# Performance work log

Measured on AMD Instinct MI355X. Metric: run time of the kernel, lower is better.

## Reference

```python
import jax, jax.numpy as jnp
import numpy as np

BN_EPS = 1e-5


def _bn(x, gamma, beta):
    # BatchNorm1d in training mode: batch mean, biased variance
    m = jnp.mean(x, axis=0)
    v = jnp.var(x, axis=0)
    return (x - m) * jax.lax.rsqrt(v + BN_EPS) * gamma + beta


def _gin_rel(h_src, h_dst, src, dst, W1, W2, g1, b1, g2, b2):
    # GINConv (eps=0): sum-aggregate src features onto dst, add self feature
    n_dst = h_dst.shape[0]
    agg = jax.ops.segment_sum(h_src[src], dst, num_segments=n_dst)  # [N_dst, d]
    x = h_dst + agg
    # MLP: Linear -> BN -> ReLU -> Linear  (both Linears bias=False)
    h = jax.nn.relu(_bn(x @ W1, g1, b1)) @ W2
    # GINBase: BN -> ReLU
    return jax.nn.relu(_bn(h, g2, b2))


def setup_inputs() -> dict:
    key = jax.random.key(0)
    ks = jax.random.split(key, 12)
    N_U, N_I, E, D = 50000, 50000, 640000, 128
    s = 1.0 / np.sqrt(D)
    inp = {
        "h_user": jax.random.normal(ks[0], (N_U, D), jnp.float32),
        "h_item": jax.random.normal(ks[1], (N_I, D), jnp.float32),
        "src_rates": jax.random.randint(ks[2], (E,), 0, N_U, jnp.int32),
        "dst_rates": jax.random.randint(ks[3], (E,), 0, N_I, jnp.int32),
        "src_rev": jax.random.randint(ks[4], (E,), 0, N_I, jnp.int32),
        "dst_rev": jax.random.randint(ks[5], (E,), 0, N_U, jnp.int32),
        "W1_rates": jax.random.normal(ks[6], (D, D), jnp.float32) * s,
        "W2_rates": jax.random.normal(ks[7], (D, D), jnp.float32) * s,
        "g1_rates": jnp.ones((D,), jnp.float32),
        "b1_rates": jnp.zeros((D,), jnp.float32),
        "g2_rates": jnp.ones((D,), jnp.float32),
        "b2_rates": jnp.zeros((D,), jnp.float32),
        "W1_rev": jax.random.normal(ks[8], (D, D), jnp.float32) * s,
        "W2_rev": jax.random.normal(ks[9], (D, D), jnp.float32) * s,
        "g1_rev": jnp.ones((D,), jnp.float32),
        "b1_rev": jnp.zeros((D,), jnp.float32),
        "g2_rev": jnp.ones((D,), jnp.float32),
        "b2_rev": jnp.zeros((D,), jnp.float32),
    }
    return inp


def reference(h_user, h_item, src_rates, dst_rates, src_rev, dst_rev,
              W1_rates, W2_rates, g1_rates, b1_rates, g2_rates, b2_rates,
              W1_rev, W2_rev, g1_rev, b1_rev, g2_rev, b2_rev):
    # relation 'rates': user -> item; relation 'rated_by': item -> user
    out_item = _gin_rel(h_user, h_item, src_rates, dst_rates,
                        W1_rates, W2_rates, g1_rates, b1_rates, g2_rates, b2_rates)
    out_user = _gin_rel(h_item, h_user, src_rev, dst_rev,
                        W1_rev, W2_rev, g1_rev, b1_rev, g2_rev, b2_rev)
    # HeteroGraphConv sums per dst type; one relation per dst type here.
    # GINLayer squeezes each output (no-op for 2D tensors).
    return (out_user, out_item)
```

## Files before the change

kernel.cpp:

```cpp
#include <hip/hip_runtime.h>

#define D 128
#define NBUK 4
#define NCHF 128
#define FILL_FINE 1024
#define MAXT 4
#define FUSE_GX 256
static constexpr float BN_EPS = 1e-5f;

typedef __attribute__((ext_vector_type(8))) short short8;
typedef __attribute__((ext_vector_type(4))) float f32x4;

__device__ __forceinline__ unsigned short f2bf(float f)
{
    unsigned u = __builtin_bit_cast(unsigned, f);
    unsigned r = u + 0x7fffu + ((u >> 16) & 1u);
    return (unsigned short)(r >> 16);
}
__device__ __forceinline__ float bflo(unsigned u)
{
    return __builtin_bit_cast(float, u << 16);
}
__device__ __forceinline__ float bfhi(unsigned u)
{
    return __builtin_bit_cast(float, u & 0xffff0000u);
}

struct CsrRel {
    const int* src; const int* dst;
    int* counts; int* offsets; int* bsum; int* perm;
    unsigned char* rank8; unsigned* pc;
    int E; int N; int nscan;
};
struct GatherRel {
    const unsigned short* hb;
    const unsigned short* hbd;
    const int* offsets; const int* perm;
    unsigned short* x; int N;
};
struct FusedRel {
    const unsigned short* X;
    const unsigned short* Wt1;
    const unsigned short* Wt2;
    const float* g1; const float* b1; const float* g2; const float* b2;
    float* st;
    float* out;
    int N; int ntiles;
};

__global__ __launch_bounds__(256) void prep_kernel(
    const float* __restrict__ hu, const float* __restrict__ hi,
    unsigned short* __restrict__ bu, unsigned short* __restrict__ bi8,
    int nu8, int ni8,
    const float* __restrict__ Wa, const float* __restrict__ Wb,
    const float* __restrict__ Wc, const float* __restrict__ Wd,
    unsigned short* __restrict__ wt, float* __restrict__ stats,
    int* __restrict__ bar)
{
    const int t = threadIdx.x;
    if (blockIdx.x < 64) {
        const int wsel = blockIdx.x >> 4;
        const float* W = wsel == 0 ? Wa : wsel == 1 ? Wb : wsel == 2 ? Wc : Wd;
        unsigned short* out = wt + (size_t)wsel * D * D;
        const int tile = blockIdx.x & 15;
        const int k0 = (tile >> 2) * 32, n0 = (tile & 3) * 32;
        __shared__ float s[32][33];
        const int r = t >> 3, c = (t & 7) * 4;
        float4 v = *reinterpret_cast<const float4*>(W + (size_t)(k0 + r) * D + n0 + c);
        s[r][c] = v.x; s[r][c + 1] = v.y; s[r][c + 2] = v.z; s[r][c + 3] = v.w;
        __syncthreads();
        unsigned lo = (unsigned)f2bf(s[c][r]) | ((unsigned)f2bf(s[c + 1][r]) << 16);
        unsigned hi = (unsigned)f2bf(s[c + 2][r]) | ((unsigned)f2bf(s[c + 3][r]) << 16);
        *reinterpret_cast<uint2*>(out + (size_t)(n0 + r) * D + k0 + c) =
            make_uint2(lo, hi);
        return;
    }
    if (blockIdx.x == 64) {
        reinterpret_cast<float4*>(stats)[t] = make_float4(0.f, 0.f, 0.f, 0.f);
        if (t < 8) bar[t] = 0;
        return;
    }
    int i = (blockIdx.x - 65) * 256 + t;
    if (i >= nu8 + ni8) return;
    const float* s; unsigned short* d; int o;
    if (i < nu8) { s = hu; d = bu; o = i; }
    else         { s = hi; d = bi8; o = i - nu8; }
    float4 v0 = reinterpret_cast<const float4*>(s)[o * 2];
    float4 v1 = reinterpret_cast<const float4*>(s)[o * 2 + 1];
    uint4 r;
    r.x = (unsigned)f2bf(v0.x) | ((unsigned)f2bf(v0.y) << 16);
    r.y = (unsigned)f2bf(v0.z) | ((unsigned)f2bf(v0.w) << 16);
    r.z = (unsigned)f2bf(v1.x) | ((unsigned)f2bf(v1.y) << 16);
    r.w = (unsigned)f2bf(v1.z) | ((unsigned)f2bf(v1.w) << 16);
    reinterpret_cast<uint4*>(d)[o] = r;
}

__global__ __launch_bounds__(256) void hist_kernel(CsrRel r0, CsrRel r1)
{
    CsrRel r = blockIdx.y ? r1 : r0;
    extern __shared__ unsigned h4[];
    const int t = threadIdx.x;
    const int c = blockIdx.x;
    const int CE = (r.E + NCHF - 1) / NCHF;
    const int e0 = c * CE;
    const int e1 = min(e0 + CE, r.E);
    const int bw4 = (r.N + 3) >> 2;

    for (int i = t; i < bw4; i += 256) h4[i] = 0u;
    __syncthreads();
    for (int e = e0 + t; e < e1; e += 256) {
        int d = r.dst[e];
        unsigned sh = (unsigned)(d & 3) * 8u;
        unsigned old = atomicAdd(&h4[d >> 2], 1u << sh);
        r.rank8[e] = (unsigned char)((old >> sh) & 0xffu);
    }
    __syncthreads();
    unsigned* out = r.pc + (size_t)c * bw4;
    for (int i = t; i < bw4; i += 256) out[i] = h4[i];
}

__global__ __launch_bounds__(256) void chunkpfx_kernel(CsrRel r0, CsrRel r1)
{
    CsrRel r = blockIdx.y ? r1 : r0;
    __shared__ unsigned lds[NCHF * 256];
    const int t = threadIdx.x;
    const int j = blockIdx.x * 256 + t;
    const int bw4 = (r.N + 3) >> 2;
    int s = 0;
    if (j < bw4) {
        const unsigned* base = r.pc + j;
#pragma unroll 4
        for (int c = 0; c < NCHF; ++c)
            lds[c * 256 + t] = base[(size_t)c * bw4];
        unsigned s0 = 0, s1 = 0, s2 = 0, s3 = 0;
        for (int c = 0; c < NCHF; ++c) {
            unsigned v = lds[c * 256 + t];
            lds[c * 256 + t] = s0 | (s1 << 8) | (s2 << 16) | (s3 << 24);
            s0 += v & 0xffu;
            s1 += (v >> 8) & 0xffu;
            s2 += (v >> 16) & 0xffu;
            s3 += v >> 24;
        }
        unsigned* wb = r.pc + j;
#pragma unroll 4
        for (int c = 0; c < NCHF; ++c)
            wb[(size_t)c * bw4] = lds[c * 256 + t];
        int d0 = 4 * j;
        r.counts[d0] = (int)s0;
        if (d0 + 1 < r.N) r.counts[d0 + 1] = (int)s1;
        if (d0 + 2 < r.N) r.counts[d0 + 2] = (int)s2;
        if (d0 + 3 < r.N) r.counts[d0 + 3] = (int)s3;
        s = (int)(s0 + s1 + s2 + s3);
    }
    __shared__ int red[256];
    red[t] = s;
    __syncthreads();
    for (int off = 128; off > 0; off >>= 1) {
        if (t < off) red[t] += red[t + off];
        __syncthreads();
    }
    if (t == 0) r.bsum[blockIdx.x] = red[0];
}

__global__ __launch_bounds__(256) void scan_offsets_kernel(CsrRel rr0, CsrRel rr1)
{
    CsrRel r = blockIdx.y ? rr1 : rr0;
    if ((int)blockIdx.x >= r.nscan) return;
    __shared__ int pb[64];
    __shared__ int part[256];
    const int t = threadIdx.x;
    if (t == 0) {
        int run = 0;
        for (int i = 0; i < r.nscan; ++i) { pb[i] = run; run += r.bsum[i]; }
    }
    const int d0 = blockIdx.x * 1024 + t * 4;
    int v0 = 0, v1 = 0, v2 = 0, v3 = 0;
    if (d0 + 3 < r.N) {
        int4 q = *reinterpret_cast<const int4*>(r.counts + d0);
        v0 = q.x; v1 = q.y; v2 = q.z; v3 = q.w;
    } else {
        if (d0 < r.N) v0 = r.counts[d0];
        if (d0 + 1 < r.N) v1 = r.counts[d0 + 1];
        if (d0 + 2 < r.N) v2 = r.counts[d0 + 2];
        if (d0 + 3 < r.N) v3 = r.counts[d0 + 3];
    }
    int s = v0 + v1 + v2 + v3;
    part[t] = s;
    __syncthreads();
    for (int off = 1; off < 256; off <<= 1) {
        int tmp = (t >= off) ? part[t - off] : 0;
        __syncthreads();
        part[t] += tmp;
        __syncthreads();
    }
    int excl = part[t] - s + pb[blockIdx.x];
    int o0 = excl, o1 = o0 + v0, o2 = o1 + v1, o3 = o2 + v2;
    if (d0 + 3 < r.N) {
        *reinterpret_cast<int4*>(r.offsets + d0) = make_int4(o0, o1, o2, o3);
    } else {
        if (d0 < r.N) r.offsets[d0] = o0;
        if (d0 + 1 < r.N) r.offsets[d0 + 1] = o1;
        if (d0 + 2 < r.N) r.offsets[d0 + 2] = o2;
        if (d0 + 3 < r.N) r.offsets[d0 + 3] = o3;
    }
    if (d0 < r.N && d0 + 4 >= r.N) r.offsets[r.N] = excl + s;
}

__global__ __launch_bounds__(256) void fill_kernel(CsrRel rr0, CsrRel rr1)
{
    CsrRel r = blockIdx.y ? rr1 : rr0;
    const int b = blockIdx.x & (NBUK - 1);
    const int fc = blockIdx.x >> 2;
    const int f0 = fc * FILL_FINE;
    if (f0 >= r.E) return;
    const int f1 = min(f0 + FILL_FINE, r.E);
    const int bw = (r.N + NBUK - 1) / NBUK;
    const int lo = b * bw;
    const int hi = min(lo + bw, r.N);
    const int CE = (r.E + NCHF - 1) / NCHF;
    const int c0 = f0 / CE;
    const int cb = (c0 + 1) * CE;
    const int bw4 = (r.N + 3) >> 2;
    const unsigned* pcb0 = r.pc + (size_t)c0 * bw4;
    const unsigned* pcb1 = pcb0 + bw4;
    for (int e = f0 + threadIdx.x; e < f1; e += 256) {
        int d = r.dst[e];
        if (d >= lo && d < hi) {
            const unsigned* pcc = (e >= cb) ? pcb1 : pcb0;
            unsigned sh = (unsigned)(d & 3) * 8u;
            int px = (int)((pcc[d >> 2] >> sh) & 0xffu);
            r.perm[r.offsets[d] + px + (int)r.rank8[e]] = r.src[e];
        }
    }
}

__global__ __launch_bounds__(256) void gather_agg_kernel(GatherRel g0, GatherRel g1)
{
    GatherRel g = blockIdx.y ? g1 : g0;
    int row = blockIdx.x * 4 + (threadIdx.x >> 6);
    row = __builtin_amdgcn_readfirstlane(row);
    if (row >= g.N) return;
    const int c = (threadIdx.x & 63) * 2;
    const int beg = g.offsets[row], end = g.offsets[row + 1];
    unsigned us = *reinterpret_cast<const unsigned*>(g.hbd + (size_t)row * D + c);
    float2 acc = make_float2(bflo(us), bfhi(us));
    const unsigned short* hb = g.hb;
    int i = beg;
    for (; i + 7 < end; i += 8) {
        unsigned u[8];
#pragma unroll
        for (int k = 0; k < 8; ++k) {
            int s = g.perm[i + k];
            u[k] = *reinterpret_cast<const unsigned*>(hb + (size_t)s * D + c);
        }
        float ax = 0.f, ay = 0.f;
#pragma unroll
        for (int k = 0; k < 8; ++k) { ax += bflo(u[k]); ay += bfhi(u[k]); }
        acc.x += ax;
        acc.y += ay;
    }
    if (i + 3 < end) {
        int s0 = g.perm[i], s1 = g.perm[i + 1];
        int s2 = g.perm[i + 2], s3 = g.perm[i + 3];
        unsigned u0 = *reinterpret_cast<const unsigned*>(hb + (size_t)s0 * D + c);
        unsigned u1 = *reinterpret_cast<const unsigned*>(hb + (size_t)s1 * D + c);
        unsigned u2 = *reinterpret_cast<const unsigned*>(hb + (size_t)s2 * D + c);
        unsigned u3 = *reinterpret_cast<const unsigned*>(hb + (size_t)s3 * D + c);
        acc.x += (bflo(u0) + bflo(u1)) + (bflo(u2) + bflo(u3));
        acc.y += (bfhi(u0) + bfhi(u1)) + (bfhi(u2) + bfhi(u3));
        i += 4;
    }
    for (; i < end; ++i) {
        unsigned u = *reinterpret_cast<const unsigned*>(hb + (size_t)g.perm[i] * D + c);
        acc.x += bflo(u);
        acc.y += bfhi(u);
    }
    unsigned o = (unsigned)f2bf(acc.x) | ((unsigned)f2bf(acc.y) << 16);
    *reinterpret_cast<unsigned*>(g.x + (size_t)row * D + c) = o;
}

__device__ __forceinline__ unsigned bnpack(unsigned u, float sLo, float sHi,
                                           float bLo, float bHi)
{
    float lo = fmaxf(fmaf(bflo(u), sLo, bLo), 0.f);
    float hi = fmaxf(fmaf(bfhi(u), sHi, bHi), 0.f);
    return (unsigned)f2bf(lo) | ((unsigned)f2bf(hi) << 16);
}

__device__ __forceinline__ void rel_barrier(int* ctr)
{
    __syncthreads();
    if (threadIdx.x == 0) {
        __hip_atomic_fetch_add(ctr, 1, __ATOMIC_RELAXED, __HIP_MEMORY_SCOPE_AGENT);
        while (__hip_atomic_load(ctr, __ATOMIC_RELAXED, __HIP_MEMORY_SCOPE_AGENT)
               < FUSE_GX)
            __builtin_amdgcn_s_sleep(2);
        int v = __hip_atomic_load(ctr, __ATOMIC_ACQUIRE, __HIP_MEMORY_SCOPE_AGENT);
        asm volatile("" :: "s"(v));
    }
    __syncthreads();
}

__device__ __forceinline__ float ld_atomic(const float* p)
{
    return __hip_atomic_load(p, __ATOMIC_RELAXED, __HIP_MEMORY_SCOPE_AGENT);
}

__global__ __launch_bounds__(256, 2) void fused_mlp_kernel(FusedRel q0, FusedRel q1,
                                                           int* bar)
{
    FusedRel q = blockIdx.y ? q1 : q0;
    int* bA = bar + blockIdx.y * 2;
    __shared__ unsigned short ylds[MAXT * 64 * D];
    __shared__ float s_sc[D], s_bi[D];
    __shared__ float ssum[4][D], ssq[4][D];
    char* yb = reinterpret_cast<char*>(ylds);

    const int t = threadIdx.x;
    const int w = t >> 6;
    const int l = t & 63;
    const int lr = l & 15;
    const int lk = (l >> 4) << 3;

    uint4 wf[4][8];
    float ps[8], pq[8];

#pragma unroll
    for (int kk = 0; kk < 4; ++kk)
#pragma unroll
        for (int n = 0; n < 8; ++n)
            wf[kk][n] = *reinterpret_cast<const uint4*>(
                q.Wt1 + (size_t)(n * 16 + lr) * D + kk * 32 + lk);
#pragma unroll
    for (int n = 0; n < 8; ++n) { ps[n] = 0.f; pq[n] = 0.f; }

    for (int mt = 0; mt < MAXT; ++mt) {
        int tile = (int)blockIdx.x + mt * FUSE_GX;
        if (tile >= q.ntiles) break;
        f32x4 acc[8];
#pragma unroll
        for (int n = 0; n < 8; ++n) acc[n] = (f32x4){0.f, 0.f, 0.f, 0.f};
        const int arow = tile * 64 + w * 16 + lr;
#pragma unroll
        for (int kk = 0; kk < 4; ++kk) {
            uint4 a4 = make_uint4(0u, 0u, 0u, 0u);
            if (arow < q.N)
                a4 = *reinterpret_cast<const uint4*>(
                    q.X + (size_t)arow * D + kk * 32 + lk);
            short8 a = __builtin_bit_cast(short8, a4);
#pragma unroll
            for (int n = 0; n < 8; ++n)
                acc[n] = __builtin_amdgcn_mfma_f32_16x16x32_bf16(
                    a, __builtin_bit_cast(short8, wf[kk][n]), acc[n], 0, 0, 0);
        }
        const int lrow = w * 16 + ((l >> 4) << 2);
#pragma unroll
        for (int n = 0; n < 8; ++n) {
#pragma unroll
            for (int j = 0; j < 4; ++j) {
                float v = acc[n][j];
                ps[n] += v;
                pq[n] += v * v;
                int row = lrow + j;
                int by = (((row << 8) + ((n * 16 + lr) << 1)) ^ ((row & 7) << 4));
                *reinterpret_cast<unsigned short*>(yb + mt * 16384 + by) = f2bf(v);
            }
        }
    }
#pragma unroll
    for (int n = 0; n < 8; ++n) {
        ps[n] += __shfl_xor(ps[n], 16); ps[n] += __shfl_xor(ps[n], 32);
        pq[n] += __shfl_xor(pq[n], 16); pq[n] += __shfl_xor(pq[n], 32);
    }
    if (l < 16) {
#pragma unroll
        for (int n = 0; n < 8; ++n) {
            ssum[w][n * 16 + l] = ps[n];
            ssq[w][n * 16 + l]  = pq[n];
        }
    }
    __syncthreads();
    if (t < D) {
        atomicAdd(&q.st[t], ssum[0][t] + ssum[1][t] + ssum[2][t] + ssum[3][t]);
        atomicAdd(&q.st[D + t], ssq[0][t] + ssq[1][t] + ssq[2][t] + ssq[3][t]);
    }
    rel_barrier(bA);

    if (t < D) {
        float inv_n = 1.f / (float)q.N;
        float mean = ld_atomic(&q.st[t]) * inv_n;
        float var = fmaxf(ld_atomic(&q.st[D + t]) * inv_n - mean * mean, 0.f);
        float s = q.g1[t] * rsqrtf(var + BN_EPS);
        s_sc[t] = s;
        s_bi[t] = q.b1[t] - mean * s;
    }
    __syncthreads();
#pragma unroll
    for (int kk = 0; kk < 4; ++kk)
#pragma unroll
        for (int n = 0; n < 8; ++n)
            wf[kk][n] = *reinterpret_cast<const uint4*>(
                q.Wt2 + (size_t)(n * 16 + lr) * D + kk * 32 + lk);
#pragma unroll
    for (int n = 0; n < 8; ++n) { ps[n] = 0.f; pq[n] = 0.f; }

    for (int mt = 0; mt < MAXT; ++mt) {
        int tile = (int)blockIdx.x + mt * FUSE_GX;
        if (tile >= q.ntiles) break;
        f32x4 acc[8];
#pragma unroll
        for (int n = 0; n < 8; ++n) acc[n] = (f32x4){0.f, 0.f, 0.f, 0.f};
        const int yrow = w * 16 + lr;
        const int grow = tile * 64 + yrow;
#pragma unroll
        for (int kk = 0; kk < 4; ++kk) {
            uint4 a4 = make_uint4(0u, 0u, 0u, 0u);
            if (grow < q.N) {
                int by = (((yrow << 8) + ((kk * 32 + lk) << 1)) ^ ((yrow & 7) << 4));
                a4 = *reinterpret_cast<const uint4*>(yb + mt * 16384 + by);
                const int kb = kk * 32 + lk;
                float4 s0 = *reinterpret_cast<const float4*>(&s_sc[kb]);
                float4 s1 = *reinterpret_cast<const float4*>(&s_sc[kb + 4]);
                float4 b0 = *reinterpret_cast<const float4*>(&s_bi[kb]);
                float4 b1 = *reinterpret_cast<const float4*>(&s_bi[kb + 4]);
                a4.x = bnpack(a4.x, s0.x, s0.y, b0.x, b0.y);
                a4.y = bnpack(a4.y, s0.z, s0.w, b0.z, b0.w);
                a4.z = bnpack(a4.z, s1.x, s1.y, b1.x, b1.y);
                a4.w = bnpack(a4.w, s1.z, s1.w, b1.z, b1.w);
            }
            short8 a = __builtin_bit_cast(short8, a4);
#pragma unroll
            for (int n = 0; n < 8; ++n)
                acc[n] = __builtin_amdgcn_mfma_f32_16x16x32_bf16(
                    a, __builtin_bit_cast(short8, wf[kk][n]), acc[n], 0, 0, 0);
        }
        const int lrow = w * 16 + ((l >> 4) << 2);
#pragma unroll
        for (int n = 0; n < 8; ++n) {
#pragma unroll
            for (int j = 0; j < 4; ++j) {
                float v = acc[n][j];
                ps[n] += v;
                pq[n] += v * v;
                int row = lrow + j;
                int by = (((row << 8) + ((n * 16 + lr) << 1)) ^ ((row & 7) << 4));
                *reinterpret_cast<unsigned short*>(yb + mt * 16384 + by) = f2bf(v);
            }
        }
    }
#pragma unroll
    for (int n = 0; n < 8; ++n) {
        ps[n] += __shfl_xor(ps[n], 16); ps[n] += __shfl_xor(ps[n], 32);
        pq[n] += __shfl_xor(pq[n], 16); pq[n] += __shfl_xor(pq[n], 32);
    }
    __syncthreads();
    if (l < 16) {
#pragma unroll
        for (int n = 0; n < 8; ++n) {
            ssum[w][n * 16 + l] = ps[n];
            ssq[w][n * 16 + l]  = pq[n];
        }
    }
    __syncthreads();
    if (t < D) {
        atomicAdd(&q.st[2 * D + t], ssum[0][t] + ssum[1][t] + ssum[2][t] + ssum[3][t]);
        atomicAdd(&q.st[3 * D + t], ssq[0][t] + ssq[1][t] + ssq[2][t] + ssq[3][t]);
    }
    rel_barrier(bA + 1);

    if (t < D) {
        float inv_n = 1.f / (float)q.N;
        float mean = ld_atomic(&q.st[2 * D + t]) * inv_n;
        float var = fmaxf(ld_atomic(&q.st[3 * D + t]) * inv_n - mean * mean, 0.f);
        float s = q.g2[t] * rsqrtf(var + BN_EPS);
        s_sc[t] = s;
        s_bi[t] = q.b2[t] - mean * s;
    }
    __syncthreads();
    const float sc0 = s_sc[2 * l], sc1 = s_sc[2 * l + 1];
    const float bi0 = s_bi[2 * l], bi1 = s_bi[2 * l + 1];
    for (int mt = 0; mt < MAXT; ++mt) {
        int tile = (int)blockIdx.x + mt * FUSE_GX;
        if (tile >= q.ntiles) break;
#pragma unroll
        for (int rr = 0; rr < 16; ++rr) {
            int row = w * 16 + rr;
            int grow = tile * 64 + row;
            if (grow >= q.N) break;
            int by = (((row << 8) + (l << 2)) ^ ((row & 7) << 4));
            unsigned u = *reinterpret_cast<const unsigned*>(yb + mt * 16384 + by);
            float2 o;
            o.x = fmaxf(fmaf(bflo(u), sc0, bi0), 0.f);
            o.y = fmaxf(fmaf(bfhi(u), sc1, bi1), 0.f);
            *reinterpret_cast<float2*>(q.out + (size_t)grow * D + 2 * l) = o;
        }
    }
}

extern "C" void kernel_launch(void* const* d_in, const int* in_sizes, int n_in,
                              void* d_out, int out_size, void* d_ws, size_t ws_size,
                              hipStream_t stream)
{
    const float* h_user   = (const float*)d_in[0];
    const float* h_item   = (const float*)d_in[1];
    const int* src_rates  = (const int*)d_in[2];
    const int* dst_rates  = (const int*)d_in[3];
    const int* src_rev    = (const int*)d_in[4];
    const int* dst_rev    = (const int*)d_in[5];
    const float* W1_rates = (const float*)d_in[6];
    const float* W2_rates = (const float*)d_in[7];
    const float* g1_rates = (const float*)d_in[8];
    const float* b1_rates = (const float*)d_in[9];
    const float* g2_rates = (const float*)d_in[10];
    const float* b2_rates = (const float*)d_in[11];
    const float* W1_rev   = (const float*)d_in[12];
    const float* W2_rev   = (const float*)d_in[13];
    const float* g1_rev   = (const float*)d_in[14];
    const float* b1_rev   = (const float*)d_in[15];
    const float* g2_rev   = (const float*)d_in[16];
    const float* b2_rev   = (const float*)d_in[17];

    const int n_user = in_sizes[0] / D;
    const int n_item = in_sizes[1] / D;
    const int E1 = in_sizes[2];
    const int E2 = in_sizes[4];

    const int bw4_0 = (n_item + 3) >> 2;
    const int bw4_1 = (n_user + 3) >> 2;

    char* p = (char*)d_ws;
    auto alloc = [&](size_t bytes) {
        char* q = p;
        p += (bytes + 255) & ~(size_t)255;
        return q;
    };
    unsigned short* hbu = (unsigned short*)alloc((size_t)n_user * D * 2);
    unsigned short* hbi = (unsigned short*)alloc((size_t)n_item * D * 2);
    unsigned short* xz0 = (unsigned short*)alloc((size_t)n_item * D * 2);
    unsigned short* xz1 = (unsigned short*)alloc((size_t)n_user * D * 2);
    unsigned short* wt  = (unsigned short*)alloc((size_t)4 * D * D * 2);
    float* stats   = (float*)alloc((size_t)8 * D * 4);
    int* bar       = (int*)alloc((size_t)8 * 4);
    int* counts0   = (int*)alloc((size_t)n_item * 4);
    int* counts1   = (int*)alloc((size_t)n_user * 4);
    int* offsets0  = (int*)alloc(((size_t)n_item + 1) * 4);
    int* offsets1  = (int*)alloc(((size_t)n_user + 1) * 4);
    int* bsum0     = (int*)alloc((size_t)64 * 4);
    int* bsum1     = (int*)alloc((size_t)64 * 4);
    int* perm0     = (int*)alloc((size_t)E1 * 4);
    int* perm1     = (int*)alloc((size_t)E2 * 4);
    unsigned char* rank0 = (unsigned char*)alloc((size_t)E1);
    unsigned char* rank1 = (unsigned char*)alloc((size_t)E2);
    unsigned* pc0  = (unsigned*)alloc((size_t)NCHF * bw4_0 * 4);
    unsigned* pc1  = (unsigned*)alloc((size_t)NCHF * bw4_1 * 4);

    float* out_user = (float*)d_out;
    float* out_item = out_user + (size_t)n_user * D;

    const int nu8 = n_user * D / 8, ni8 = n_item * D / 8;
    int pblocks = 65 + (nu8 + ni8 + 255) / 256;
    prep_kernel<<<pblocks, 256, 0, stream>>>(
        h_user, h_item, hbu, hbi, nu8, ni8,
        W1_rates, W2_rates, W1_rev, W2_rev, wt, stats, bar);

    float* st0 = stats;
    float* st1 = stats + 4 * D;

    CsrRel c0 = {src_rates, dst_rates, counts0, offsets0, bsum0, perm0,
                 rank0, pc0, E1, n_item, (n_item + 1023) / 1024};
    CsrRel c1 = {src_rev, dst_rev, counts1, offsets1, bsum1, perm1,
                 rank1, pc1, E2, n_user, (n_user + 1023) / 1024};

    int nmax = n_item > n_user ? n_item : n_user;
    int emax = E1 > E2 ? E1 : E2;
    int bw4m = bw4_0 > bw4_1 ? bw4_0 : bw4_1;
    int ns = c0.nscan > c1.nscan ? c0.nscan : c1.nscan;

    size_t hist_lds = (size_t)bw4m * 4;
    hist_kernel<<<dim3(NCHF, 2), 256, hist_lds, stream>>>(c0, c1);
    chunkpfx_kernel<<<dim3((bw4m + 255) / 256, 2), 256, 0, stream>>>(c0, c1);
    scan_offsets_kernel<<<dim3(ns, 2), 256, 0, stream>>>(c0, c1);
    int nfine = (emax + FILL_FINE - 1) / FILL_FINE;
    fill_kernel<<<dim3(NBUK * nfine, 2), 256, 0, stream>>>(c0, c1);

    GatherRel ga0 = {hbu, hbi, offsets0, perm0, xz0, n_item};
    GatherRel ga1 = {hbi, hbu, offsets1, perm1, xz1, n_user};
    int ab = (nmax + 3) / 4;
    gather_agg_kernel<<<dim3(ab, 2), 256, 0, stream>>>(ga0, ga1);

    const int nt0 = (n_item + 63) / 64, nt1 = (n_user + 63) / 64;
    FusedRel f0 = {xz0, wt,             wt + (size_t)D * D,
                   g1_rates, b1_rates, g2_rates, b2_rates,
                   st0, out_item, n_item, nt0};
    FusedRel f1 = {xz1, wt + (size_t)2 * D * D, wt + (size_t)3 * D * D,
                   g1_rev, b1_rev, g2_rev, b2_rev,
                   st1, out_user, n_user, nt1};
    fused_mlp_kernel<<<dim3(FUSE_GX, 2), 256, 0, stream>>>(f0, f1, bar);
}
```

Before: 184.6 us.

## Spread BN stat atomics over slots, prefetch X tiles and W2 before barrier

BatchNorm statistics atomics now go to 16 separate partial-sum slots chosen by block index instead of one shared array, which reduces contention on the same addresses. Each block sums the 16 slots after the grid barrier. All X tiles for the first GEMM are loaded up front into registers, the W2 fragments are loaded before the barrier so that latency hides behind the wait, and the tile loops are unrolled. The extra registers may lower occupancy or cause spills, and the slot reduction adds more loads after each barrier.

```diff
diff --git a/kernel.cpp b/kernel.cpp
--- a/kernel.cpp
+++ b/kernel.cpp
@@ -6,6 +6,7 @@
 #define FILL_FINE 1024
 #define MAXT 4
 #define FUSE_GX 256
+#define NACC 16
 static constexpr float BN_EPS = 1e-5f;
 
 typedef __attribute__((ext_vector_type(8))) short short8;
@@ -43,7 +44,8 @@
     const unsigned short* Wt1;
     const unsigned short* Wt2;
     const float* g1; const float* b1; const float* g2; const float* b2;
-    float* st;
+    float* pb1;
+    float* pb2;
     float* out;
     int N; int ntiles;
 };
@@ -54,7 +56,7 @@
     int nu8, int ni8,
     const float* __restrict__ Wa, const float* __restrict__ Wb,
     const float* __restrict__ Wc, const float* __restrict__ Wd,
-    unsigned short* __restrict__ wt, float* __restrict__ stats,
+    unsigned short* __restrict__ wt, float* __restrict__ pbAll,
     int* __restrict__ bar)
 {
     const int t = threadIdx.x;
@@ -76,7 +78,10 @@
         return;
     }
     if (blockIdx.x == 64) {
-        reinterpret_cast<float4*>(stats)[t] = make_float4(0.f, 0.f, 0.f, 0.f);
+        float4 z4 = make_float4(0.f, 0.f, 0.f, 0.f);
+        const int n4 = 4 * NACC * 256 / 4;
+        for (int i = t; i < n4; i += 256)
+            reinterpret_cast<float4*>(pbAll)[i] = z4;
         if (t < 8) bar[t] = 0;
         return;
     }
@@ -301,11 +306,6 @@
     __syncthreads();
 }
 
-__device__ __forceinline__ float ld_atomic(const float* p)
-{
-    return __hip_atomic_load(p, __ATOMIC_RELAXED, __HIP_MEMORY_SCOPE_AGENT);
-}
-
 __global__ __launch_bounds__(256, 2) void fused_mlp_kernel(FusedRel q0, FusedRel q1,
                                                            int* bar)
 {
@@ -313,6 +313,7 @@
     int* bA = bar + blockIdx.y * 2;
     __shared__ unsigned short ylds[MAXT * 64 * D];
     __shared__ float s_sc[D], s_bi[D];
+    __shared__ float s_red[256];
     __shared__ float ssum[4][D], ssq[4][D];
     char* yb = reinterpret_cast<char*>(ylds);
 
@@ -321,6 +322,7 @@
     const int l = t & 63;
     const int lr = l & 15;
     const int lk = (l >> 4) << 3;
+    const int accrow = ((int)blockIdx.x & (NACC - 1)) * 256;
 
     uint4 wf[4][8];
     float ps[8], pq[8];
@@ -334,20 +336,30 @@
 #pragma unroll
     for (int n = 0; n < 8; ++n) { ps[n] = 0.f; pq[n] = 0.f; }
 
+    uint4 xa[MAXT][4];
+#pragma unroll
+    for (int mt = 0; mt < MAXT; ++mt) {
+        const int tile = (int)blockIdx.x + mt * FUSE_GX;
+        const int arow = tile * 64 + w * 16 + lr;
+#pragma unroll
+        for (int kk = 0; kk < 4; ++kk) {
+            xa[mt][kk] = make_uint4(0u, 0u, 0u, 0u);
+            if (tile < q.ntiles && arow < q.N)
+                xa[mt][kk] = *reinterpret_cast<const uint4*>(
+                    q.X + (size_t)arow * D + kk * 32 + lk);
+        }
+    }
+
+#pragma unroll
     for (int mt = 0; mt < MAXT; ++mt) {
         int tile = (int)blockIdx.x + mt * FUSE_GX;
         if (tile >= q.ntiles) break;
         f32x4 acc[8];
 #pragma unroll
         for (int n = 0; n < 8; ++n) acc[n] = (f32x4){0.f, 0.f, 0.f, 0.f};
-        const int arow = tile * 64 + w * 16 + lr;
 #pragma unroll
         for (int kk = 0; kk < 4; ++kk) {
-            uint4 a4 = make_uint4(0u, 0u, 0u, 0u);
-            if (arow < q.N)
-                a4 = *reinterpret_cast<const uint4*>(
-                    q.X + (size_t)arow * D + kk * 32 + lk);
-            short8 a = __builtin_bit_cast(short8, a4);
+            short8 a = __builtin_bit_cast(short8, xa[mt][kk]);
 #pragma unroll
             for (int n = 0; n < 8; ++n)
                 acc[n] = __builtin_amdgcn_mfma_f32_16x16x32_bf16(
@@ -381,29 +393,41 @@
     }
     __syncthreads();
     if (t < D) {
-        atomicAdd(&q.st[t], ssum[0][t] + ssum[1][t] + ssum[2][t] + ssum[3][t]);
-        atomicAdd(&q.st[D + t], ssq[0][t] + ssq[1][t] + ssq[2][t] + ssq[3][t]);
-    }
+        atomicAdd(&q.pb1[accrow + t],
+                  ssum[0][t] + ssum[1][t] + ssum[2][t] + ssum[3][t]);
+        atomicAdd(&q.pb1[accrow + D + t],
+                  ssq[0][t] + ssq[1][t] + ssq[2][t] + ssq[3][t]);
+    }
+#pragma unroll
+    for (int kk = 0; kk < 4; ++kk)
+#pragma unroll
+        for (int n = 0; n < 8; ++n)
+            wf[kk][n] = *reinterpret_cast<const uint4*>(
+                q.Wt2 + (size_t)(n * 16 + lr) * D + kk * 32 + lk);
     rel_barrier(bA);
 
+    {
+        float acc = 0.f;
+#pragma unroll
+        for (int b = 0; b < NACC; ++b)
+            acc += __hip_atomic_load(q.pb1 + b * 256 + t, __ATOMIC_RELAXED,
+                                     __HIP_MEMORY_SCOPE_AGENT);
+        s_red[t] = acc;
+    }
+    __syncthreads();
     if (t < D) {
         float inv_n = 1.f / (float)q.N;
-        float mean = ld_atomic(&q.st[t]) * inv_n;
-        float var = fmaxf(ld_atomic(&q.st[D + t]) * inv_n - mean * mean, 0.f);
+        float mean = s_red[t] * inv_n;
+        float var = fmaxf(s_red[D + t] * inv_n - mean * mean, 0.f);
         float s = q.g1[t] * rsqrtf(var + BN_EPS);
         s_sc[t] = s;
         s_bi[t] = q.b1[t] - mean * s;
     }
     __syncthreads();
 #pragma unroll
-    for (int kk = 0; kk < 4; ++kk)
-#pragma unroll
-        for (int n = 0; n < 8; ++n)
-            wf[kk][n] = *reinterpret_cast<const uint4*>(
-                q.Wt2 + (size_t)(n * 16 + lr) * D + kk * 32 + lk);
-#pragma unroll
     for (int n = 0; n < 8; ++n) { ps[n] = 0.f; pq[n] = 0.f; }
 
+#pragma unroll
     for (int mt = 0; mt < MAXT; ++mt) {
         int tile = (int)blockIdx.x + mt * FUSE_GX;
         if (tile >= q.ntiles) break;
@@ -463,15 +487,26 @@
     }
     __syncthreads();
     if (t < D) {
-        atomicAdd(&q.st[2 * D + t], ssum[0][t] + ssum[1][t] + ssum[2][t] + ssum[3][t]);
-        atomicAdd(&q.st[3 * D + t], ssq[0][t] + ssq[1][t] + ssq[2][t] + ssq[3][t]);
+        atomicAdd(&q.pb2[accrow + t],
+                  ssum[0][t] + ssum[1][t] + ssum[2][t] + ssum[3][t]);
+        atomicAdd(&q.pb2[accrow + D + t],
+                  ssq[0][t] + ssq[1][t] + ssq[2][t] + ssq[3][t]);
     }
     rel_barrier(bA + 1);
 
+    {
+        float acc = 0.f;
+#pragma unroll
+        for (int b = 0; b < NACC; ++b)
+            acc += __hip_atomic_load(q.pb2 + b * 256 + t, __ATOMIC_RELAXED,
+                                     __HIP_MEMORY_SCOPE_AGENT);
+        s_red[t] = acc;
+    }
+    __syncthreads();
     if (t < D) {
         float inv_n = 1.f / (float)q.N;
-        float mean = ld_atomic(&q.st[2 * D + t]) * inv_n;
-        float var = fmaxf(ld_atomic(&q.st[3 * D + t]) * inv_n - mean * mean, 0.f);
+        float mean = s_red[t] * inv_n;
+        float var = fmaxf(s_red[D + t] * inv_n - mean * mean, 0.f);
         float s = q.g2[t] * rsqrtf(var + BN_EPS);
         s_sc[t] = s;
         s_bi[t] = q.b2[t] - mean * s;
@@ -479,6 +514,7 @@
     __syncthreads();
     const float sc0 = s_sc[2 * l], sc1 = s_sc[2 * l + 1];
     const float bi0 = s_bi[2 * l], bi1 = s_bi[2 * l + 1];
+#pragma unroll
     for (int mt = 0; mt < MAXT; ++mt) {
         int tile = (int)blockIdx.x + mt * FUSE_GX;
         if (tile >= q.ntiles) break;
@@ -539,7 +575,7 @@
     unsigned short* xz0 = (unsigned short*)alloc((size_t)n_item * D * 2);
     unsigned short* xz1 = (unsigned short*)alloc((size_t)n_user * D * 2);
     unsigned short* wt  = (unsigned short*)alloc((size_t)4 * D * D * 2);
-    float* stats   = (float*)alloc((size_t)8 * D * 4);
+    float* pbAll   = (float*)alloc((size_t)4 * NACC * 256 * 4);
     int* bar       = (int*)alloc((size_t)8 * 4);
     int* counts0   = (int*)alloc((size_t)n_item * 4);
     int* counts1   = (int*)alloc((size_t)n_user * 4);
@@ -561,10 +597,7 @@
     int pblocks = 65 + (nu8 + ni8 + 255) / 256;
     prep_kernel<<<pblocks, 256, 0, stream>>>(
         h_user, h_item, hbu, hbi, nu8, ni8,
-        W1_rates, W2_rates, W1_rev, W2_rev, wt, stats, bar);
-
-    float* st0 = stats;
-    float* st1 = stats + 4 * D;
+        W1_rates, W2_rates, W1_rev, W2_rev, wt, pbAll, bar);
 
     CsrRel c0 = {src_rates, dst_rates, counts0, offsets0, bsum0, perm0,
                  rank0, pc0, E1, n_item, (n_item + 1023) / 1024};
@@ -591,9 +624,11 @@
     const int nt0 = (n_item + 63) / 64, nt1 = (n_user + 63) / 64;
     FusedRel f0 = {xz0, wt,             wt + (size_t)D * D,
                    g1_rates, b1_rates, g2_rates, b2_rates,
-                   st0, out_item, n_item, nt0};
+                   pbAll,            pbAll + NACC * 256,
+                   out_item, n_item, nt0};
     FusedRel f1 = {xz1, wt + (size_t)2 * D * D, wt + (size_t)3 * D * D,
                    g1_rev, b1_rev, g2_rev, b2_rev,
-                   st1, out_user, n_user, nt1};
+                   pbAll + 2 * NACC * 256, pbAll + 3 * NACC * 256,
+                   out_user, n_user, nt1};
     fused_mlp_kernel<<<dim3(FUSE_GX, 2), 256, 0, stream>>>(f0, f1, bar);
 }
```

New measurement: 188.7 us. +2.2%, slower.
